# Performance work log

Hardware: AMD Instinct MI355X
Metric: run time of the kernel (lower is better)

## Reference

```python
import jax, jax.numpy as jnp
import numpy as np

EPS = 1e-12  # matches torch F.normalize default eps in spectral_norm


def _l2norm(v):
    return v / jnp.maximum(jnp.linalg.norm(v), EPS)


def _spectral_norm(W, u):
    # One power-iteration step (torch spectral_norm training behavior).
    # u, v are treated as constants w.r.t. gradients.
    v = jax.lax.stop_gradient(_l2norm(W.T @ u))
    u2 = jax.lax.stop_gradient(_l2norm(W @ v))
    sigma = jnp.einsum('o,oi,i->', u2, W, v)
    return W / sigma


def setup_inputs() -> dict:
    key = jax.random.key(0)
    ks = jax.random.split(key, 8)
    B, C, N = 8, 512, 2048
    d = C // 8
    return {
        'x':  jax.random.normal(ks[0], (B, C, N), dtype=jnp.float32),
        'Wq': jax.random.normal(ks[1], (d, C), dtype=jnp.float32) * (1.0 / np.sqrt(C)),
        'Wk': jax.random.normal(ks[2], (d, C), dtype=jnp.float32) * (1.0 / np.sqrt(C)),
        'Wv': jax.random.normal(ks[3], (C, C), dtype=jnp.float32) * (1.0 / np.sqrt(C)),
        'uq': jax.random.normal(ks[4], (d,), dtype=jnp.float32),
        'uk': jax.random.normal(ks[5], (d,), dtype=jnp.float32),
        'uv': jax.random.normal(ks[6], (C,), dtype=jnp.float32),
        'gamma': jax.random.normal(ks[7], (1,), dtype=jnp.float32) * 0.1,
    }


def reference(x, Wq, Wk, Wv, uq, uk, uv, gamma):
    # x: [B, C, N]
    f = jnp.einsum('oi,bin->bon', _spectral_norm(Wq, uq), x)  # [B, C/8, N]
    g = jnp.einsum('oi,bin->bon', _spectral_norm(Wk, uk), x)  # [B, C/8, N]
    h = jnp.einsum('oi,bin->bon', _spectral_norm(Wv, uv), x)  # [B, C, N]
    scores = jnp.einsum('bdn,bdm->bnm', f, g)                 # f^T g: [B, N, N]
    beta = jax.nn.softmax(scores, axis=1)                      # softmax over dim=1
    o = gamma[0] * jnp.einsum('bcn,bnm->bcm', h, beta) + x    # [B, C, N]
    return o
```

## Files before the change

### kernel.cpp

```cpp
#include <hip/hip_runtime.h>
#include <hip/hip_bf16.h>
#include <math.h>

#define B_ 8
#define C_ 512
#define N_ 2048
#define D_ 64
#define O_ 640

typedef __bf16 bf16x8 __attribute__((ext_vector_type(8)));
typedef float f32x4 __attribute__((ext_vector_type(4)));
typedef unsigned short ushort8_t __attribute__((ext_vector_type(8)));
typedef unsigned short ushort4_t __attribute__((ext_vector_type(4)));

__device__ __forceinline__ unsigned short f2bf(float f) {
    unsigned int u = __builtin_bit_cast(unsigned int, f);
    u += 0x7fffu + ((u >> 16) & 1u);
    return (unsigned short)(u >> 16);
}

__device__ __forceinline__ unsigned short f2bf_hw(float f) {
    __bf16 h = (__bf16)f;
    return __builtin_bit_cast(unsigned short, h);
}

__device__ __forceinline__ float fastexp(float x) {
    return exp2f(x * 1.44269504088896340736f);
}

union FragU { ushort8_t u; bf16x8 b; };

__device__ __forceinline__ bf16x8 ldfrag(const unsigned short* p) {
    FragU t; t.u = *(const ushort8_t*)p; return t.b;
}

__device__ __forceinline__ void gload_lds16(const unsigned short* g, unsigned short* l) {
    __builtin_amdgcn_global_load_lds((const __attribute__((address_space(1))) void*)g,
                                     (__attribute__((address_space(3))) void*)l,
                                     16, 0, 0);
}

__global__ __launch_bounds__(512) void k_colvec(const float* __restrict__ Wq,
                                                const float* __restrict__ Wk,
                                                const float* __restrict__ Wv,
                                                const float* __restrict__ uq,
                                                const float* __restrict__ uk,
                                                const float* __restrict__ uv,
                                                float* __restrict__ tpart) {
    int which = blockIdx.y, oq = blockIdx.x;
    const float* W; const float* u; int R;
    if (which == 0)      { W = Wq; u = uq; R = 64;  }
    else if (which == 1) { W = Wk; u = uk; R = 64;  }
    else                 { W = Wv; u = uv; R = 512; }
    int chunk = R >> 2;
    int i = threadIdx.x;
    float s = 0.f;
    int o0 = oq * chunk, o1 = o0 + chunk;
    for (int o = o0; o < o1; ++o) s += W[(size_t)o * 512 + i] * u[o];
    tpart[((which << 2) + oq) * 512 + i] = s;
}

__global__ __launch_bounds__(512) void k_trow(const float* __restrict__ tpart,
                                              float* __restrict__ tvec,
                                              float* __restrict__ t2) {
    int which = blockIdx.x, i = threadIdx.x;
    const float* tp = tpart + (which << 2) * 512;
    float s = tp[i] + tp[512 + i] + tp[1024 + i] + tp[1536 + i];
    tvec[which * 512 + i] = s;
    __shared__ float red[512];
    red[i] = s * s; __syncthreads();
    for (int st = 256; st > 0; st >>= 1) { if (i < st) red[i] += red[i + st]; __syncthreads(); }
    if (i == 0) t2[which] = red[0];
}

__global__ __launch_bounds__(256) void k_rowvec(const float* __restrict__ Wq,
                                                const float* __restrict__ Wk,
                                                const float* __restrict__ Wv,
                                                const float* __restrict__ tvec,
                                                float* __restrict__ wpart) {
    int which = blockIdx.y;
    const float* W; int R;
    if (which == 0)      { W = Wq; R = 64;  }
    else if (which == 1) { W = Wk; R = 64;  }
    else                 { W = Wv; R = 512; }
    int tid = threadIdx.x, lane = tid & 63, wv = tid >> 6;
    int row = blockIdx.x * 4 + wv;
    float ps = 0.f;
    if (row < R) {
        const float4* wr_ = (const float4*)(W + (size_t)row * 512);
        const float4* tv = (const float4*)(tvec + which * 512);
        float4 a0 = wr_[lane * 2], a1 = wr_[lane * 2 + 1];
        float4 b0 = tv[lane * 2], b1 = tv[lane * 2 + 1];
        float s = a0.x * b0.x + a0.y * b0.y + a0.z * b0.z + a0.w * b0.w
                + a1.x * b1.x + a1.y * b1.y + a1.z * b1.z + a1.w * b1.w;
        #pragma unroll
        for (int off = 1; off < 64; off <<= 1) s += __shfl_xor(s, off, 64);
        ps = s * s;
    }
    __shared__ float red[4];
    if (lane == 0) red[wv] = ps;
    __syncthreads();
    if (tid == 0) wpart[which * 128 + blockIdx.x] = red[0] + red[1] + red[2] + red[3];
}

__global__ __launch_bounds__(128) void k_scale(const float* __restrict__ wpart,
                                               const float* __restrict__ t2,
                                               float* __restrict__ scales) {
    int which = blockIdx.x, tid = threadIdx.x;
    float s = wpart[which * 128 + tid];
    #pragma unroll
    for (int off = 1; off < 64; off <<= 1) s += __shfl_xor(s, off, 64);
    __shared__ float r2[2];
    if ((tid & 63) == 0) r2[tid >> 6] = s;
    __syncthreads();
    if (tid == 0) scales[which] = sqrtf(t2[which] / fmaxf(r2[0] + r2[1], 1e-24f));
}

__global__ __launch_bounds__(256) void k_wconv(const float* __restrict__ Wq,
                                               const float* __restrict__ Wk,
                                               const float* __restrict__ Wv,
                                               const float* __restrict__ scales,
                                               unsigned short* __restrict__ Wb) {
    int gid = blockIdx.x * 256 + threadIdx.x;
    int e0 = gid * 8;
    int o = e0 >> 9, i = e0 & 511;
    const float* src; float sc;
    if (o < 64)       { src = Wq + (size_t)o * 512;         sc = scales[0]; }
    else if (o < 128) { src = Wk + (size_t)(o - 64) * 512;  sc = scales[1]; }
    else              { src = Wv + (size_t)(o - 128) * 512; sc = scales[2]; }
    float4 v0 = *(const float4*)(src + i), v1 = *(const float4*)(src + i + 4);
    ushort8_t u;
    u[0] = f2bf(v0.x * sc); u[1] = f2bf(v0.y * sc); u[2] = f2bf(v0.z * sc); u[3] = f2bf(v0.w * sc);
    u[4] = f2bf(v1.x * sc); u[5] = f2bf(v1.y * sc); u[6] = f2bf(v1.z * sc); u[7] = f2bf(v1.w * sc);
    *(ushort8_t*)&Wb[(size_t)o * 512 + i] = u;
}

__global__ __launch_bounds__(256) void k_transpose(const float* __restrict__ x,
                                                   unsigned short* __restrict__ xT) {
    __shared__ float tile[64][33];
    int b = blockIdx.z;
    int n0 = blockIdx.x * 32, c0 = blockIdx.y * 64;
    int tx = threadIdx.x, ty = threadIdx.y;
    #pragma unroll
    for (int k = 0; k < 8; ++k) {
        int c = ty + k * 8;
        tile[c][tx] = x[((size_t)b * C_ + c0 + c) * N_ + n0 + tx];
    }
    __syncthreads();
    #pragma unroll
    for (int k = 0; k < 4; ++k) {
        int n = ty + k * 8;
        unsigned int p = (unsigned int)f2bf(tile[tx * 2][n]) |
                         ((unsigned int)f2bf(tile[tx * 2 + 1][n]) << 16);
        *(unsigned int*)&xT[((size_t)b * N_ + n0 + n) * C_ + c0 + tx * 2] = p;
    }
}

__global__ __launch_bounds__(256) void k_proj(const unsigned short* __restrict__ xT,
                                              const unsigned short* __restrict__ Wb,
                                              unsigned short* __restrict__ fT,
                                              unsigned short* __restrict__ gT,
                                              unsigned short* __restrict__ hb) {
    int b = blockIdx.z, n0 = blockIdx.y * 128, o0 = blockIdx.x * 128;
    int tid = threadIdx.x, lane = tid & 63, w = tid >> 6;
    int wr = w >> 1, wc = w & 1;
    __shared__ __align__(16) unsigned short Sh[16384];
    unsigned short* As = Sh;
    unsigned short* Bs = Sh + 8192;
    f32x4 zero = {0.f, 0.f, 0.f, 0.f};
    f32x4 acc[4][4];
    #pragma unroll
    for (int i = 0; i < 4; ++i)
        #pragma unroll
        for (int j = 0; j < 4; ++j) acc[i][j] = zero;
    int r8 = lane >> 3, s = lane & 7;
    int scol = (s ^ r8) * 8;

    for (int kt = 0; kt < 8; ++kt) {
        #pragma unroll
        for (int q = 0; q < 4; ++q) {
            int chunk = w * 4 + q;
            int row = chunk * 8 + r8;
            gload_lds16(xT + ((size_t)b * N_ + n0 + row) * C_ + kt * 64 + scol, &As[chunk * 512]);
            gload_lds16(Wb + (size_t)(o0 + row) * C_ + kt * 64 + scol, &Bs[chunk * 512]);
        }
        __syncthreads();
        int kg = lane >> 4, r16 = lane & 15;
        #pragma unroll
        for (int kk = 0; kk < 2; ++kk) {
            int sw = kk * 4 + kg;
            bf16x8 af[4];
            #pragma unroll
            for (int i = 0; i < 4; ++i) {
                int row = wr * 64 + i * 16 + r16;
                af[i] = ldfrag(&As[row * 64 + (sw ^ (row & 7)) * 8]);
            }
            #pragma unroll
            for (int j = 0; j < 4; ++j) {
                int row = wc * 64 + j * 16 + r16;
                bf16x8 bv = ldfrag(&Bs[row * 64 + (sw ^ (row & 7)) * 8]);
                #pragma unroll
                for (int i = 0; i < 4; ++i)
                    acc[i][j] = __builtin_amdgcn_mfma_f32_16x16x32_bf16(af[i], bv, acc[i][j], 0, 0, 0);
            }
        }
        __syncthreads();
    }

    unsigned short* St = Sh;
    if (o0 == 0) {
        #pragma unroll
        for (int p = 0; p < 2; ++p) {
            if (wc == p) {
                #pragma unroll
                for (int i = 0; i < 4; ++i)
                    #pragma unroll
                    for (int j = 0; j < 4; ++j)
                        #pragma unroll
                        for (int r = 0; r < 4; ++r)
                            St[(wr * 64 + i * 16 + (lane >> 4) * 4 + r) * 72 + j * 16 + (lane & 15)] = f2bf(acc[i][j][r]);
            }
            __syncthreads();
            unsigned short* dst = p == 0 ? fT : gT;
            #pragma unroll
            for (int it = 0; it < 4; ++it) {
                int row = it * 32 + (tid >> 3);
                *(ushort8_t*)&dst[((size_t)b * N_ + n0 + row) * D_ + (tid & 7) * 8] =
                    *(ushort8_t*)&St[row * 72 + (tid & 7) * 8];
            }
            __syncthreads();
        }
    } else {
        int ho0 = o0 - 128;
        #pragma unroll
        for (int p = 0; p < 2; ++p) {
            if (wc == p) {
                #pragma unroll
                for (int i = 0; i < 4; ++i)
                    #pragma unroll
                    for (int j = 0; j < 4; ++j)
                        #pragma unroll
                        for (int r = 0; r < 4; ++r)
                            St[(j * 16 + (lane & 15)) * 136 + wr * 64 + i * 16 + (lane >> 4) * 4 + r] = f2bf(acc[i][j][r]);
            }
            __syncthreads();
            #pragma unroll
            for (int it = 0; it < 4; ++it) {
                int row = it * 16 + (tid >> 4);
                *(ushort8_t*)&hb[((size_t)b * C_ + ho0 + p * 64 + row) * N_ + n0 + (tid & 15) * 8] =
                    *(ushort8_t*)&St[row * 136 + (tid & 15) * 8];
            }
            __syncthreads();
        }
    }
}

__global__ __launch_bounds__(256) void k_stats(const unsigned short* __restrict__ fT,
                                               const unsigned short* __restrict__ gT,
                                               float* __restrict__ colmax,
                                               float* __restrict__ colsinv) {
    int b = blockIdx.y, m0 = blockIdx.x * 16;
    int tid = threadIdx.x, lane = tid & 63, w = tid >> 6;
    int mcol = m0 + (lane & 15);
    const unsigned short* gbase = gT + ((size_t)b * N_ + mcol) * D_ + (lane >> 4) * 8;
    bf16x8 g0 = ldfrag(gbase);
    bf16x8 g1 = ldfrag(gbase + 32);

    float mx = -1e30f, sm = 0.f;
    for (int nt = w * 32; nt < w * 32 + 32; ++nt) {
        const unsigned short* abase = fT + ((size_t)b * N_ + nt * 16 + (lane & 15)) * D_ + (lane >> 4) * 8;
        f32x4 s = {0.f, 0.f, 0.f, 0.f};
        s = __builtin_amdgcn_mfma_f32_16x16x32_bf16(ldfrag(abase), g0, s, 0, 0, 0);
        s = __builtin_amdgcn_mfma_f32_16x16x32_bf16(ldfrag(abase + 32), g1, s, 0, 0, 0);
        float tm = fmaxf(fmaxf(s[0], s[1]), fmaxf(s[2], s[3]));
        float nm = fmaxf(mx, tm);
        float c = fastexp(mx - nm);
        sm = sm * c + fastexp(s[0] - nm) + fastexp(s[1] - nm) + fastexp(s[2] - nm) + fastexp(s[3] - nm);
        mx = nm;
    }
    #pragma unroll
    for (int off = 16; off < 64; off <<= 1) {
        float omx = __shfl_xor(mx, off, 64);
        float osm = __shfl_xor(sm, off, 64);
        float nm = fmaxf(mx, omx);
        sm = sm * fastexp(mx - nm) + osm * fastexp(omx - nm);
        mx = nm;
    }
    __shared__ float lmx[4][16], lsm[4][16];
    if ((lane >> 4) == 0) { lmx[w][lane & 15] = mx; lsm[w][lane & 15] = sm; }
    __syncthreads();
    if (tid < 16) {
        float M = lmx[0][tid], S = lsm[0][tid];
        #pragma unroll
        for (int q = 1; q < 4; ++q) {
            float om = lmx[q][tid], os = lsm[q][tid];
            float nm = fmaxf(M, om);
            S = S * fastexp(M - nm) + os * fastexp(om - nm);
            M = nm;
        }
        colmax[(size_t)b * N_ + m0 + tid] = M;
        colsinv[(size_t)b * N_ + m0 + tid] = 1.0f / S;
    }
}

__global__ __launch_bounds__(512, 4) void k_av(const unsigned short* __restrict__ fT,
                                               const unsigned short* __restrict__ gT,
                                               const unsigned short* __restrict__ hb,
                                               const float* __restrict__ colmax,
                                               const float* __restrict__ colsinv,
                                               const float* __restrict__ x,
                                               const float* __restrict__ gamma,
                                               float* __restrict__ out) {
    __shared__ __align__(16) unsigned short FT[2][4096];
    __shared__ __align__(16) unsigned short HB[2][8192];
    __shared__ __align__(16) unsigned short BS[8192];

    int bid = blockIdx.x;
    int xg = bid & 7, sidx = bid >> 3;
    int mi = sidx & 15, gh = sidx >> 4;
    int g = xg + 8 * gh;
    int b = g >> 2, cq = g & 3;
    int m0 = mi * 128, c0 = cq * 128;

    int tid = threadIdx.x, lane = tid & 63, w = tid >> 6;
    int nw = w & 3, mh = w >> 2;
    int l15 = lane & 15, lq = lane >> 4;
    int r8 = lane >> 3, sl = lane & 7;
    int scol = (sl ^ r8) * 8;

    bf16x8 gf[4][2];
    float mx_[4], siv_[4];
    #pragma unroll
    for (int j = 0; j < 4; ++j) {
        int m = m0 + mh * 64 + j * 16 + l15;
        #pragma unroll
        for (int kd = 0; kd < 2; ++kd)
            gf[j][kd] = ldfrag(gT + ((size_t)b * N_ + m) * D_ + kd * 32 + lq * 8);
        mx_[j] = colmax[(size_t)b * N_ + m];
        siv_[j] = colsinv[(size_t)b * N_ + m];
    }

    f32x4 zero = {0.f, 0.f, 0.f, 0.f};
    f32x4 acc[4][2];
    #pragma unroll
    for (int i = 0; i < 4; ++i)
        #pragma unroll
        for (int j = 0; j < 2; ++j) acc[i][j] = zero;

    const unsigned short* fbase = fT + ((size_t)b * N_) * D_;
    const unsigned short* hbase = hb + ((size_t)b * C_ + c0) * N_;

    {
        gload_lds16(fbase + (size_t)(w * 8 + r8) * D_ + scol, &FT[0][w * 512]);
        #pragma unroll
        for (int q = 0; q < 2; ++q) {
            int ci = w * 2 + q;
            gload_lds16(hbase + (size_t)(ci * 8 + r8) * N_ + scol, &HB[0][ci * 512]);
        }
    }

    int buf = 0;
    for (int kt = 0; kt < N_ / 64; ++kt) {
        __syncthreads();

        int arow = nw * 16 + l15;
        bf16x8 af0 = ldfrag(&FT[buf][arow * 64 + ((lq ^ (arow & 7)) * 8)]);
        bf16x8 af1 = ldfrag(&FT[buf][arow * 64 + (((4 + lq) ^ (arow & 7)) * 8)]);
        #pragma unroll
        for (int j = 0; j < 4; ++j) {
            f32x4 sv = zero;
            sv = __builtin_amdgcn_mfma_f32_16x16x32_bf16(af0, gf[j][0], sv, 0, 0, 0);
            sv = __builtin_amdgcn_mfma_f32_16x16x32_bf16(af1, gf[j][1], sv, 0, 0, 0);
            int mrel = mh * 64 + j * 16 + l15;
            ushort4_t pk;
            #pragma unroll
            for (int r = 0; r < 4; ++r)
                pk[r] = f2bf_hw(fastexp(sv[r] - mx_[j]) * siv_[j]);
            int nt = nw * 16 + lq * 4;
            *(ushort4_t*)&BS[mrel * 64 + (((nt >> 3) ^ (mrel & 7)) * 8) + (nt & 7)] = pk;
        }
        __syncthreads();

        if (kt + 1 < N_ / 64) {
            int nb = buf ^ 1;
            gload_lds16(fbase + ((size_t)(kt + 1) * 64 + w * 8 + r8) * D_ + scol, &FT[nb][w * 512]);
            #pragma unroll
            for (int q = 0; q < 2; ++q) {
                int ci = w * 2 + q;
                gload_lds16(hbase + (size_t)(ci * 8 + r8) * N_ + (kt + 1) * 64 + scol, &HB[nb][ci * 512]);
            }
        }

        __builtin_amdgcn_s_setprio(1);
        #pragma unroll
        for (int kk = 0; kk < 2; ++kk) {
            int ng = kk * 4 + lq;
            bf16x8 pa[4];
            #pragma unroll
            for (int i = 0; i < 4; ++i) {
                int mr = mh * 64 + i * 16 + l15;
                pa[i] = ldfrag(&BS[mr * 64 + ((ng ^ (mr & 7)) * 8)]);
            }
            #pragma unroll
            for (int j = 0; j < 2; ++j) {
                int cr = nw * 32 + j * 16 + l15;
                bf16x8 hv = ldfrag(&HB[buf][cr * 64 + ((ng ^ (cr & 7)) * 8)]);
                #pragma unroll
                for (int i = 0; i < 4; ++i)
                    acc[i][j] = __builtin_amdgcn_mfma_f32_16x16x32_bf16(pa[i], hv, acc[i][j], 0, 0, 0);
            }
        }
        __builtin_amdgcn_s_setprio(0);
        buf ^= 1;
    }

    float gv = gamma[0];
    #pragma unroll
    for (int i = 0; i < 4; ++i) {
        int mabs = m0 + mh * 64 + i * 16 + lq * 4;
        #pragma unroll
        for (int j = 0; j < 2; ++j) {
            int cabs = c0 + nw * 32 + j * 16 + l15;
            size_t base = ((size_t)b * C_ + cabs) * N_ + mabs;
            float4 xv = *(const float4*)(x + base);
            float4 ov;
            ov.x = gv * acc[i][j][0] + xv.x;
            ov.y = gv * acc[i][j][1] + xv.y;
            ov.z = gv * acc[i][j][2] + xv.z;
            ov.w = gv * acc[i][j][3] + xv.w;
            *(float4*)(out + base) = ov;
        }
    }
}

extern "C" void kernel_launch(void* const* d_in, const int* in_sizes, int n_in,
                              void* d_out, int out_size, void* d_ws, size_t ws_size,
                              hipStream_t stream) {
    const float* x     = (const float*)d_in[0];
    const float* Wq    = (const float*)d_in[1];
    const float* Wk    = (const float*)d_in[2];
    const float* Wv    = (const float*)d_in[3];
    const float* uq    = (const float*)d_in[4];
    const float* uk    = (const float*)d_in[5];
    const float* uv    = (const float*)d_in[6];
    const float* gamma = (const float*)d_in[7];
    float* out = (float*)d_out;

    char* wsb = (char*)d_ws;
    float* scales         = (float*)wsb;
    unsigned short* xT    = (unsigned short*)(wsb + 256);
    unsigned short* fT    = xT + (size_t)B_ * N_ * C_;
    unsigned short* gT    = fT + (size_t)B_ * N_ * D_;
    unsigned short* hb    = gT + (size_t)B_ * N_ * D_;
    float* colmax         = (float*)(hb + (size_t)B_ * C_ * N_);
    float* colsinv        = colmax + (size_t)B_ * N_;
    float* tpart          = colsinv + (size_t)B_ * N_;
    float* tvec           = tpart + 3 * 4 * 512;
    float* t2             = tvec + 3 * 512;
    float* wpart          = t2 + 16;
    unsigned short* Wb    = (unsigned short*)(wpart + 3 * 128);

    k_colvec<<<dim3(4, 3), 512, 0, stream>>>(Wq, Wk, Wv, uq, uk, uv, tpart);
    k_trow<<<3, 512, 0, stream>>>(tpart, tvec, t2);
    k_rowvec<<<dim3(128, 3), 256, 0, stream>>>(Wq, Wk, Wv, tvec, wpart);
    k_scale<<<3, 128, 0, stream>>>(wpart, t2, scales);
    k_wconv<<<O_ * C_ / (256 * 8), 256, 0, stream>>>(Wq, Wk, Wv, scales, Wb);
    k_transpose<<<dim3(N_ / 32, C_ / 64, B_), dim3(32, 8), 0, stream>>>(x, xT);
    k_proj<<<dim3(O_ / 128, N_ / 128, B_), 256, 0, stream>>>(xT, Wb, fT, gT, hb);
    k_stats<<<dim3(N_ / 16, B_), 256, 0, stream>>>(fT, gT, colmax, colsinv);
    k_av<<<512, 512, 0, stream>>>(fT, gT, hb, colmax, colsinv, x, gamma, out);
}
```

Measured before the change: 192.0 us.

## Software-pipeline k_av with double-buffered score tile and two-ahead prefetch

Result: no change. 188.7 us (-1.7%).

```diff
diff --git a/kernel.cpp b/kernel.cpp
--- a/kernel.cpp
+++ b/kernel.cpp
@@ -313,8 +313,9 @@
                                                float* __restrict__ out) {
     __shared__ __align__(16) unsigned short FT[2][4096];
     __shared__ __align__(16) unsigned short HB[2][8192];
-    __shared__ __align__(16) unsigned short BS[8192];
-
+    __shared__ __align__(16) unsigned short BS[2][8192];
+
+    const int NT = N_ / 64;
     int bid = blockIdx.x;
     int xg = bid & 7, sidx = bid >> 3;
     int mi = sidx & 15, gh = sidx >> 4;
@@ -328,15 +329,16 @@
     int r8 = lane >> 3, sl = lane & 7;
     int scol = (sl ^ r8) * 8;
 
+    const float LOG2E = 1.44269504088896340736f;
     bf16x8 gf[4][2];
-    float mx_[4], siv_[4];
+    float mlneg[4], siv_[4];
     #pragma unroll
     for (int j = 0; j < 4; ++j) {
         int m = m0 + mh * 64 + j * 16 + l15;
         #pragma unroll
         for (int kd = 0; kd < 2; ++kd)
             gf[j][kd] = ldfrag(gT + ((size_t)b * N_ + m) * D_ + kd * 32 + lq * 8);
-        mx_[j] = colmax[(size_t)b * N_ + m];
+        mlneg[j] = -colmax[(size_t)b * N_ + m] * LOG2E;
         siv_[j] = colsinv[(size_t)b * N_ + m];
     }
 
@@ -350,22 +352,19 @@
     const unsigned short* fbase = fT + ((size_t)b * N_) * D_;
     const unsigned short* hbase = hb + ((size_t)b * C_ + c0) * N_;
 
-    {
-        gload_lds16(fbase + (size_t)(w * 8 + r8) * D_ + scol, &FT[0][w * 512]);
+    auto STAGE = [&](int kt, int p) {
+        gload_lds16(fbase + ((size_t)kt * 64 + w * 8 + r8) * D_ + scol, &FT[p][w * 512]);
         #pragma unroll
         for (int q = 0; q < 2; ++q) {
             int ci = w * 2 + q;
-            gload_lds16(hbase + (size_t)(ci * 8 + r8) * N_ + scol, &HB[0][ci * 512]);
-        }
-    }
-
-    int buf = 0;
-    for (int kt = 0; kt < N_ / 64; ++kt) {
-        __syncthreads();
-
+            gload_lds16(hbase + (size_t)(ci * 8 + r8) * N_ + kt * 64 + scol, &HB[p][ci * 512]);
+        }
+    };
+
+    auto SPHASE = [&](int p) {
         int arow = nw * 16 + l15;
-        bf16x8 af0 = ldfrag(&FT[buf][arow * 64 + ((lq ^ (arow & 7)) * 8)]);
-        bf16x8 af1 = ldfrag(&FT[buf][arow * 64 + (((4 + lq) ^ (arow & 7)) * 8)]);
+        bf16x8 af0 = ldfrag(&FT[p][arow * 64 + ((lq ^ (arow & 7)) * 8)]);
+        bf16x8 af1 = ldfrag(&FT[p][arow * 64 + (((4 + lq) ^ (arow & 7)) * 8)]);
         #pragma unroll
         for (int j = 0; j < 4; ++j) {
             f32x4 sv = zero;
@@ -375,22 +374,13 @@
             ushort4_t pk;
             #pragma unroll
             for (int r = 0; r < 4; ++r)
-                pk[r] = f2bf_hw(fastexp(sv[r] - mx_[j]) * siv_[j]);
+                pk[r] = f2bf_hw(exp2f(fmaf(sv[r], LOG2E, mlneg[j])) * siv_[j]);
             int nt = nw * 16 + lq * 4;
-            *(ushort4_t*)&BS[mrel * 64 + (((nt >> 3) ^ (mrel & 7)) * 8) + (nt & 7)] = pk;
-        }
-        __syncthreads();
-
-        if (kt + 1 < N_ / 64) {
-            int nb = buf ^ 1;
-            gload_lds16(fbase + ((size_t)(kt + 1) * 64 + w * 8 + r8) * D_ + scol, &FT[nb][w * 512]);
-            #pragma unroll
-            for (int q = 0; q < 2; ++q) {
-                int ci = w * 2 + q;
-                gload_lds16(hbase + (size_t)(ci * 8 + r8) * N_ + (kt + 1) * 64 + scol, &HB[nb][ci * 512]);
-            }
-        }
-
+            *(ushort4_t*)&BS[p][mrel * 64 + (((nt >> 3) ^ (mrel & 7)) * 8) + (nt & 7)] = pk;
+        }
+    };
+
+    auto PVPHASE = [&](int p) {
         __builtin_amdgcn_s_setprio(1);
         #pragma unroll
         for (int kk = 0; kk < 2; ++kk) {
@@ -399,19 +389,48 @@
             #pragma unroll
             for (int i = 0; i < 4; ++i) {
                 int mr = mh * 64 + i * 16 + l15;
-                pa[i] = ldfrag(&BS[mr * 64 + ((ng ^ (mr & 7)) * 8)]);
+                pa[i] = ldfrag(&BS[p][mr * 64 + ((ng ^ (mr & 7)) * 8)]);
             }
             #pragma unroll
             for (int j = 0; j < 2; ++j) {
                 int cr = nw * 32 + j * 16 + l15;
-                bf16x8 hv = ldfrag(&HB[buf][cr * 64 + ((ng ^ (cr & 7)) * 8)]);
+                bf16x8 hv = ldfrag(&HB[p][cr * 64 + ((ng ^ (cr & 7)) * 8)]);
                 #pragma unroll
                 for (int i = 0; i < 4; ++i)
                     acc[i][j] = __builtin_amdgcn_mfma_f32_16x16x32_bf16(pa[i], hv, acc[i][j], 0, 0, 0);
             }
         }
         __builtin_amdgcn_s_setprio(0);
-        buf ^= 1;
+    };
+
+    STAGE(0, 0);
+    STAGE(1, 1);
+    asm volatile("s_waitcnt vmcnt(3)" ::: "memory");
+    __builtin_amdgcn_sched_barrier(0);
+    __builtin_amdgcn_s_barrier();
+    __builtin_amdgcn_sched_barrier(0);
+    SPHASE(0);
+    asm volatile("s_waitcnt lgkmcnt(0)" ::: "memory");
+    __builtin_amdgcn_sched_barrier(0);
+    __builtin_amdgcn_s_barrier();
+    __builtin_amdgcn_sched_barrier(0);
+
+    #pragma unroll 1
+    for (int kt = 0; kt < NT; ++kt) {
+        int p = kt & 1;
+        PVPHASE(p);
+        if (kt + 1 < NT) {
+            asm volatile("s_waitcnt vmcnt(0)" ::: "memory");
+            __builtin_amdgcn_sched_barrier(0);
+            __builtin_amdgcn_s_barrier();
+            __builtin_amdgcn_sched_barrier(0);
+            if (kt + 2 < NT) STAGE(kt + 2, p);
+            SPHASE(p ^ 1);
+            asm volatile("s_waitcnt lgkmcnt(0)" ::: "memory");
+            __builtin_amdgcn_sched_barrier(0);
+            __builtin_amdgcn_s_barrier();
+            __builtin_amdgcn_sched_barrier(0);
+        }
     }
 
     float gv = gamma[0];
```
